# Kernel tuning notes

Hardware: AMD Instinct MI355X
Metric: run time of the kernel (lower is better)

## Reference

```python
import jax, jax.numpy as jnp
import numpy as np

EPS = 1e-6
HEADS = 4


def _gather(x, idx):
    # x: (b,n,...), idx: (b,n,k) -> (b,n,k,...)
    return jax.vmap(lambda xb, ib: xb[ib])(x, idx)


def _prenorm(f0, f1):
    # FiberNorm: layernorm on scalars, norm-based RMS normalization on vectors
    mu = jnp.mean(f0, -1, keepdims=True)
    var = jnp.var(f0, -1, keepdims=True)
    g0 = (f0 - mu) * jax.lax.rsqrt(var + EPS)
    n1 = jnp.sum(f1 * f1, -1)  # (b,n,d1) squared channel norms
    rms = jax.lax.rsqrt(jnp.mean(n1, -1, keepdims=True) + EPS)  # (b,n,1)
    g1 = f1 * rms[..., None]
    return g0, g1


def _forward(f0, f1, coords, nbr_idx, Wq0, Wq1, Wk00, Wk10, Wk01, Wk11, Wk11r,
             Wv00, Wv10, Wv01, Wv11, Wv11r, Rw1, Rb1, Rw20, Rw21, Wo0, Wo1,
             F0w1, F0w2, F1w1, F1w2):
    b, n, d0 = f0.shape
    d1 = f1.shape[2]
    k = nbr_idx.shape[-1]
    L = Wq0.shape[0]
    # equivariant basis ingredients: relative positions over neighbor graph
    rel = _gather(coords, nbr_idx) - coords[:, :, None, :]       # (b,n,k,3)
    dist = jnp.linalg.norm(rel, axis=-1, keepdims=True)          # (b,n,k,1)
    rhat = rel / (dist + EPS)                                    # (b,n,k,3)
    scale = 1.0 / np.sqrt(d0 // HEADS + 3 * (d1 // HEADS)).astype(np.float32)
    for l in range(L):
        # ---- attention block (prenorm -> TFN attention -> residual) ----
        g0, g1 = _prenorm(f0, f1)
        rh = jax.nn.gelu(dist @ Rw1[l] + Rb1[l])                 # radial MLP (b,n,k,rh)
        r0 = rh @ Rw20[l]                                        # (b,n,k,d0)
        r1 = rh @ Rw21[l]                                        # (b,n,k,d1)
        q0 = g0 @ Wq0[l]                                         # (b,n,d0)
        q1 = jnp.einsum('bncm,ce->bnem', g1, Wq1[l])             # (b,n,d1,3)
        h0 = _gather(g0, nbr_idx)                                # (b,n,k,d0)
        h1 = _gather(g1, nbr_idx)                                # (b,n,k,d1,3)
        dot1 = jnp.einsum('bnkcm,bnkm->bnkc', h1, rhat)          # deg1->deg0 basis contraction
        k0 = (h0 @ Wk00[l] + dot1 @ Wk10[l]) * r0
        v0 = (h0 @ Wv00[l] + dot1 @ Wv10[l]) * r0
        rh_e = rhat[:, :, :, None, :]                            # (b,n,k,1,3)
        k1 = (jnp.einsum('bnkc,ce->bnke', h0, Wk01[l])[..., None] * rh_e
              + jnp.einsum('bnkcm,ce->bnkem', h1, Wk11[l])
              + jnp.einsum('bnkc,ce->bnke', dot1, Wk11r[l])[..., None] * rh_e) * r1[..., None]
        v1 = (jnp.einsum('bnkc,ce->bnke', h0, Wv01[l])[..., None] * rh_e
              + jnp.einsum('bnkcm,ce->bnkem', h1, Wv11[l])
              + jnp.einsum('bnkc,ce->bnke', dot1, Wv11r[l])[..., None] * rh_e) * r1[..., None]
        # multi-head invariant attention logits over neighbors
        hq0 = q0.reshape(b, n, HEADS, -1)
        hk0 = k0.reshape(b, n, k, HEADS, -1)
        hq1 = q1.reshape(b, n, HEADS, -1, 3)
        hk1 = k1.reshape(b, n, k, HEADS, -1, 3)
        logits = (jnp.einsum('bnhc,bnkhc->bnkh', hq0, hk0)
                  + jnp.einsum('bnhcm,bnkhcm->bnkh', hq1, hk1)) * scale
        a = jax.nn.softmax(logits, axis=2)                       # over neighbors
        o0 = jnp.einsum('bnkh,bnkhc->bnhc', a, v0.reshape(b, n, k, HEADS, -1)).reshape(b, n, d0)
        o1 = jnp.einsum('bnkh,bnkhcm->bnhcm', a, v1.reshape(b, n, k, HEADS, -1, 3)).reshape(b, n, d1, 3)
        f0 = f0 + o0 @ Wo0[l]
        f1 = f1 + jnp.einsum('bncm,ce->bnem', o1, Wo1[l])
        # ---- feedforward residual block (prenorm -> fiber FF -> residual) ----
        g0, g1 = _prenorm(f0, f1)
        f0 = f0 + jax.nn.gelu(g0 @ F0w1[l]) @ F0w2[l]
        u1 = jnp.einsum('bncm,ce->bnem', g1, F1w1[l])            # (b,n,4*d1,3)
        gate = jax.nn.sigmoid(jnp.linalg.norm(u1, axis=-1))     # norm-gated equivariant nonlin
        u1 = u1 * gate[..., None]
        f1 = f1 + jnp.einsum('bnem,ef->bnfm', u1, F1w2[l])
    return jnp.concatenate([f0, f1.reshape(b, n, d1 * 3)], axis=-1)


def setup_inputs() -> dict:
    key = jax.random.key(0)
    ks = iter(jax.random.split(key, 40))
    b, n, k, d0, d1, L, rh = 2, 4096, 32, 64, 16, 2, 16
    def w(shape, fan):
        return jax.random.normal(next(ks), shape, jnp.float32) / np.sqrt(fan).astype(np.float32)
    inp = {
        'f0': jax.random.normal(next(ks), (b, n, d0), jnp.float32),
        'f1': jax.random.normal(next(ks), (b, n, d1, 3), jnp.float32),
        'coords': jax.random.normal(next(ks), (b, n, 3), jnp.float32),
        'nbr_idx': jax.random.randint(next(ks), (b, n, k), 0, n),
        'Wq0': w((L, d0, d0), d0), 'Wq1': w((L, d1, d1), d1),
        'Wk00': w((L, d0, d0), d0), 'Wk10': w((L, d1, d0), d1),
        'Wk01': w((L, d0, d1), d0), 'Wk11': w((L, d1, d1), d1), 'Wk11r': w((L, d1, d1), d1),
        'Wv00': w((L, d0, d0), d0), 'Wv10': w((L, d1, d0), d1),
        'Wv01': w((L, d0, d1), d0), 'Wv11': w((L, d1, d1), d1), 'Wv11r': w((L, d1, d1), d1),
        'Rw1': w((L, 1, rh), 1), 'Rb1': jnp.zeros((L, rh), jnp.float32),
        'Rw20': w((L, rh, d0), rh), 'Rw21': w((L, rh, d1), rh),
        'Wo0': w((L, d0, d0), d0), 'Wo1': w((L, d1, d1), d1),
        'F0w1': w((L, d0, 4 * d0), d0), 'F0w2': w((L, 4 * d0, d0), 4 * d0),
        'F1w1': w((L, d1, 4 * d1), d1), 'F1w2': w((L, 4 * d1, d1), 4 * d1),
    }
    return inp


def reference(f0, f1, coords, nbr_idx, Wq0, Wq1, Wk00, Wk10, Wk01, Wk11, Wk11r,
              Wv00, Wv10, Wv01, Wv11, Wv11r, Rw1, Rb1, Rw20, Rw21, Wo0, Wo1,
              F0w1, F0w2, F1w1, F1w2):
    return _forward(f0, f1, coords, nbr_idx, Wq0, Wq1, Wk00, Wk10, Wk01, Wk11,
                    Wk11r, Wv00, Wv10, Wv01, Wv11, Wv11r, Rw1, Rb1, Rw20, Rw21,
                    Wo0, Wo1, F0w1, F0w2, F1w1, F1w2)
```

## Files before the change

### kernel.cpp

```cpp
#include <hip/hip_runtime.h>
#include <math.h>

#define BB    2
#define NN    4096
#define KK    32
#define D0    64
#define D1    16
#define D13   48
#define RHD   16
#define NHEAD 4
#define NLAYER 2
#define EPS   1e-6f
#define SCALE 0.18898223650461363f
#define ETOT  (BB*NN*KK)

typedef float  f32x4 __attribute__((ext_vector_type(4)));
typedef short  s16x8 __attribute__((ext_vector_type(8)));
#define MFMA16(a,b,c) __builtin_amdgcn_mfma_f32_16x16x32_bf16(a,b,c,0,0,0)

__device__ __forceinline__ unsigned short f2bf(float x) {
    union { float f; unsigned u; } v; v.f = x;
    unsigned r = v.u + 0x7fffu + ((v.u >> 16) & 1u);
    return (unsigned short)(r >> 16);
}
__device__ __forceinline__ float bf2f(unsigned short h) {
    union { unsigned u; float f; } v; v.u = ((unsigned)h) << 16;
    return v.f;
}
__device__ __forceinline__ void split_bf(float x, unsigned short* hi, unsigned short* lo) {
    unsigned short h = f2bf(x);
    *hi = h;
    *lo = f2bf(x - bf2f(h));
}

__device__ __forceinline__ f32x4 mm3(s16x8 ah, s16x8 al, s16x8 bh, s16x8 bl, f32x4 c) {
    c = MFMA16(ah, bh, c);
    c = MFMA16(ah, bl, c);
    c = MFMA16(al, bh, c);
    return c;
}

__device__ __forceinline__ float wred(float v) {
    #pragma unroll
    for (int o = 32; o > 0; o >>= 1) v += __shfl_xor(v, o, 64);
    return v;
}

__device__ __forceinline__ float gelu_t(float x) {
    float x3 = x * x * x;
    return 0.5f * x * (1.0f + tanhf(0.7978845608028654f * (x + 0.044715f * x3)));
}

__global__ void geom_kernel(const float* __restrict__ coords,
                            const int* __restrict__ nbr,
                            float* __restrict__ rhat,
                            float* __restrict__ dist) {
    int e = blockIdx.x * blockDim.x + threadIdx.x;
    if (e >= ETOT) return;
    int bn = e / KK;
    int bb = bn / NN;
    int j  = nbr[e];
    const float* cs = coords + (size_t)bn * 3;
    const float* cn = coords + ((size_t)bb * NN + j) * 3;
    float rx = cn[0] - cs[0], ry = cn[1] - cs[1], rz = cn[2] - cs[2];
    float d  = sqrtf(rx * rx + ry * ry + rz * rz);
    float iv = 1.0f / (d + EPS);
    rhat[e * 3 + 0] = rx * iv;
    rhat[e * 3 + 1] = ry * iv;
    rhat[e * 3 + 2] = rz * iv;
    dist[e] = d;
}

__global__ __launch_bounds__(64) void prenorm_q_kernel(
    const float* __restrict__ f0, const float* __restrict__ f1,
    const float* __restrict__ Wq0, const float* __restrict__ Wq1,
    float* __restrict__ g1,
    float* __restrict__ q0, float* __restrict__ q1,
    unsigned short* __restrict__ g0H, unsigned short* __restrict__ g0L,
    unsigned short* __restrict__ g1mH, unsigned short* __restrict__ g1mL) {
    int node = blockIdx.x;
    int lane = threadIdx.x;
    __shared__ float g0s[D0], g1s[D13];

    float x  = f0[(size_t)node * D0 + lane];
    float mu = wred(x) * (1.0f / D0);
    float dv = x - mu;
    float var = wred(dv * dv) * (1.0f / D0);
    float g0v = dv * rsqrtf(var + EPS);
    split_bf(g0v, &g0H[(size_t)node * D0 + lane], &g0L[(size_t)node * D0 + lane]);
    g0s[lane] = g0v;

    float w = (lane < D13) ? f1[(size_t)node * D13 + lane] : 0.0f;
    float t = wred(w * w);
    float rms = rsqrtf(t * (1.0f / D1) + EPS);
    if (lane < D13) {
        float g1v = w * rms;
        g1[(size_t)node * D13 + lane] = g1v;
        g1s[lane] = g1v;
        int c = lane / 3, m = lane % 3;
        split_bf(g1v, &g1mH[(size_t)node * D13 + m * 16 + c],
                      &g1mL[(size_t)node * D13 + m * 16 + c]);
    }
    __syncthreads();

    float acc = 0.0f;
    #pragma unroll
    for (int c = 0; c < D0; c++) acc += g0s[c] * Wq0[c * D0 + lane];
    q0[(size_t)node * D0 + lane] = acc;
    if (lane < D13) {
        int e = lane / 3, m = lane % 3;
        float a1 = 0.0f;
        #pragma unroll
        for (int c = 0; c < D1; c++) a1 += g1s[c * 3 + m] * Wq1[c * D1 + e];
        q1[(size_t)node * D13 + lane] = a1;
    }
}

__global__ __launch_bounds__(256) void edge_prep_kernel(
    const int* __restrict__ nbr,
    const float* __restrict__ rhatb, const float* __restrict__ distb,
    const float* __restrict__ g1b,
    const float* __restrict__ Rw1, const float* __restrict__ Rb1,
    unsigned short* __restrict__ d1H, unsigned short* __restrict__ d1L,
    unsigned short* __restrict__ rhHg, unsigned short* __restrict__ rhLg) {
    int t = blockIdx.x * 256 + threadIdx.x;
    int e = t >> 4, c = t & 15;
    int bn = e >> 5;
    int bb = bn >> 12;
    int nj = nbr[e];
    const float* g1 = g1b + ((size_t)bb * NN + nj) * D13 + c * 3;
    float d1 = g1[0] * rhatb[e * 3] + g1[1] * rhatb[e * 3 + 1] + g1[2] * rhatb[e * 3 + 2];
    split_bf(d1, &d1H[t], &d1L[t]);
    float rh = gelu_t(distb[e] * Rw1[c] + Rb1[c]);
    split_bf(rh, &rhHg[t], &rhLg[t]);
}

__device__ __forceinline__ float B1val(int n, int k,
    const float* Wk00, const float* Wk10, const float* Wv00, const float* Wv10) {
    int nn = n & 63;
    const float* W0 = (n < 64) ? Wk00 : Wv00;
    const float* W1 = (n < 64) ? Wk10 : Wv10;
    if (k < 64) return W0[k * D0 + nn];
    if (k < 80) return W1[(k - 64) * D0 + nn];
    return 0.0f;
}
__device__ __forceinline__ float B2val(int n, int k,
    const float* Wk01, const float* Wk11, const float* Wk11r,
    const float* Wv01, const float* Wv11, const float* Wv11r) {
    if (n < 16) {
        if (k < 64) return Wk01[k * D1 + n];
        if (k < 80) return Wk11r[(k - 64) * D1 + n];
        return 0.0f;
    }
    if (n < 32) {
        int e = n - 16;
        if (k < 64) return Wv01[k * D1 + e];
        if (k < 80) return Wv11r[(k - 64) * D1 + e];
        return 0.0f;
    }
    if (n < 80) {
        int m = (n - 32) >> 4, e = (n - 32) & 15;
        if (k >= 80) { int mm = (k - 80) >> 4, c = (k - 80) & 15; if (mm == m) return Wk11[c * D1 + e]; }
        return 0.0f;
    }
    { int m = (n - 80) >> 4, e = (n - 80) & 15;
      if (k >= 80) { int mm = (k - 80) >> 4, c = (k - 80) & 15; if (mm == m) return Wv11[c * D1 + e]; }
      return 0.0f; }
}

__global__ void prep_kernel(
    const float* __restrict__ Wk00, const float* __restrict__ Wk10,
    const float* __restrict__ Wk01, const float* __restrict__ Wk11,
    const float* __restrict__ Wk11r,
    const float* __restrict__ Wv00, const float* __restrict__ Wv10,
    const float* __restrict__ Wv01, const float* __restrict__ Wv11,
    const float* __restrict__ Wv11r,
    const float* __restrict__ Rw20, const float* __restrict__ Rw21,
    unsigned short* __restrict__ B1H, unsigned short* __restrict__ B1L,
    unsigned short* __restrict__ B2H, unsigned short* __restrict__ B2L,
    unsigned short* __restrict__ R0H, unsigned short* __restrict__ R0L,
    unsigned short* __restrict__ R1H, unsigned short* __restrict__ R1L) {
    int id = blockIdx.x * 256 + threadIdx.x;
    if (id < 1536) {
        int ks = id >> 9, rem = id & 511, nt = rem >> 6, lane = rem & 63;
        int li = lane & 15, quad = lane >> 4;
        #pragma unroll
        for (int t = 0; t < 8; t++) {
            float v = B1val(nt * 16 + li, ks * 32 + quad * 8 + t, Wk00, Wk10, Wv00, Wv10);
            split_bf(v, &B1H[id * 8 + t], &B1L[id * 8 + t]);
        }
    } else if (id < 3584) {
        int id2 = id - 1536;
        int ks = id2 >> 9, rem = id2 & 511, nt = rem >> 6, lane = rem & 63;
        int li = lane & 15, quad = lane >> 4;
        #pragma unroll
        for (int t = 0; t < 8; t++) {
            float v = B2val(nt * 16 + li, ks * 32 + quad * 8 + t,
                            Wk01, Wk11, Wk11r, Wv01, Wv11, Wv11r);
            split_bf(v, &B2H[id2 * 8 + t], &B2L[id2 * 8 + t]);
        }
    } else if (id < 3840) {
        int id2 = id - 3584;
        int nt = id2 >> 6, lane = id2 & 63;
        int li = lane & 15, quad = lane >> 4;
        #pragma unroll
        for (int t = 0; t < 8; t++) {
            int k = quad * 8 + t;
            float v = (k < 16) ? Rw20[k * D0 + nt * 16 + li] : 0.0f;
            split_bf(v, &R0H[id2 * 8 + t], &R0L[id2 * 8 + t]);
        }
    } else if (id < 3904) {
        int id2 = id - 3840;
        int li = id2 & 15, quad = id2 >> 4;
        #pragma unroll
        for (int t = 0; t < 8; t++) {
            int k = quad * 8 + t;
            float v = (k < 16) ? Rw21[k * D1 + li] : 0.0f;
            split_bf(v, &R1H[id2 * 8 + t], &R1L[id2 * 8 + t]);
        }
    }
}

__global__ __launch_bounds__(64) void attn_fused_kernel(
    const int* __restrict__ nbr_idx,
    const float* __restrict__ rhatg,
    const float* __restrict__ q0g, const float* __restrict__ q1g,
    const unsigned short* __restrict__ g0H, const unsigned short* __restrict__ g0L,
    const unsigned short* __restrict__ g1mH, const unsigned short* __restrict__ g1mL,
    const unsigned short* __restrict__ d1H, const unsigned short* __restrict__ d1L,
    const unsigned short* __restrict__ rhHg, const unsigned short* __restrict__ rhLg,
    const unsigned short* __restrict__ B1H, const unsigned short* __restrict__ B1L,
    const unsigned short* __restrict__ B2H, const unsigned short* __restrict__ B2L,
    const unsigned short* __restrict__ R0H, const unsigned short* __restrict__ R0L,
    const unsigned short* __restrict__ R1H, const unsigned short* __restrict__ R1L,
    const float* __restrict__ Wo0, const float* __restrict__ Wo1,
    float* __restrict__ f0b, float* __restrict__ f1b) {

    int B0    = blockIdx.x * 64;
    int node0 = blockIdx.x * 2;
    int bb    = node0 >> 12;
    int lane  = threadIdx.x;
    int li    = lane & 15, quad = lane >> 4;
    int koff  = quad * 8;

    __shared__ float rhts[192];
    __shared__ float lgs0[64][4];
    __shared__ float lgs1[64][4];
    __shared__ float v0s[64][68];
    __shared__ float v1s[64][49];
    __shared__ float o0s[2][D0];
    __shared__ float o1s[2][D13];

    rhts[lane]       = rhatg[(size_t)B0 * 3 + lane];
    rhts[lane + 64]  = rhatg[(size_t)B0 * 3 + lane + 64];
    rhts[lane + 128] = rhatg[(size_t)B0 * 3 + lane + 128];
    __syncthreads();

    size_t em[4], nm[4];
    #pragma unroll
    for (int mt = 0; mt < 4; mt++) {
        em[mt] = (size_t)B0 + mt * 16 + li;
        nm[mt] = (size_t)bb * NN + nbr_idx[em[mt]];
    }

    #define APTRS(ks, nb, ee, PH, PL)                                              \
        const unsigned short *PH, *PL;                                             \
        if (ks < 2) {                                                              \
            PH = g0H + (nb) * 64 + ks * 32 + koff;                                 \
            PL = g0L + (nb) * 64 + ks * 32 + koff;                                 \
        } else if (ks == 2) {                                                      \
            PH = (quad < 2) ? d1H + (ee) * 16 + quad * 8                           \
                            : g1mH + (nb) * 48 + (quad - 2) * 8;                   \
            PL = (quad < 2) ? d1L + (ee) * 16 + quad * 8                           \
                            : g1mL + (nb) * 48 + (quad - 2) * 8;                   \
        } else {                                                                   \
            PH = (quad < 2) ? g1mH + (nb) * 48 + 16 + quad * 8                     \
                            : g1mH + (nb) * 48 + 32 + (quad - 2) * 8;              \
            PL = (quad < 2) ? g1mL + (nb) * 48 + 16 + quad * 8                     \
                            : g1mL + (nb) * 48 + 32 + (quad - 2) * 8;              \
        }

    f32x4 acc[4][8];

    #pragma unroll
    for (int i = 0; i < 4; i++)
        #pragma unroll
        for (int j = 0; j < 8; j++) acc[i][j] = (f32x4){0.f, 0.f, 0.f, 0.f};
    #pragma unroll
    for (int ks = 0; ks < 3; ks++) {
        s16x8 ah[4], al[4];
        #pragma unroll
        for (int mt = 0; mt < 4; mt++) {
            APTRS(ks, nm[mt], em[mt], pH, pL)
            ah[mt] = *(const s16x8*)pH;
            al[mt] = *(const s16x8*)pL;
        }
        #pragma unroll
        for (int nt = 0; nt < 8; nt++) {
            s16x8 bh = *(const s16x8*)(B1H + ((ks * 8 + nt) * 64 + lane) * 8);
            s16x8 bl = *(const s16x8*)(B1L + ((ks * 8 + nt) * 64 + lane) * 8);
            #pragma unroll
            for (int mt = 0; mt < 4; mt++)
                acc[mt][nt] = mm3(ah[mt], al[mt], bh, bl, acc[mt][nt]);
        }
    }

    {
        f32x4 r0a[4][4];
        #pragma unroll
        for (int i = 0; i < 4; i++)
            #pragma unroll
            for (int j = 0; j < 4; j++) r0a[i][j] = (f32x4){0.f, 0.f, 0.f, 0.f};
        s16x8 zz = (s16x8){0,0,0,0,0,0,0,0};
        s16x8 rah[4], ral[4];
        #pragma unroll
        for (int mt = 0; mt < 4; mt++) {
            rah[mt] = zz; ral[mt] = zz;
            if (quad < 2) {
                rah[mt] = *(const s16x8*)(rhHg + em[mt] * 16 + koff);
                ral[mt] = *(const s16x8*)(rhLg + em[mt] * 16 + koff);
            }
        }
        #pragma unroll
        for (int nt = 0; nt < 4; nt++) {
            s16x8 bh = *(const s16x8*)(R0H + (nt * 64 + lane) * 8);
            s16x8 bl = *(const s16x8*)(R0L + (nt * 64 + lane) * 8);
            #pragma unroll
            for (int mt = 0; mt < 4; mt++)
                r0a[mt][nt] = mm3(rah[mt], ral[mt], bh, bl, r0a[mt][nt]);
        }

        float q0e[2][4];
        #pragma unroll
        for (int nw = 0; nw < 2; nw++)
            #pragma unroll
            for (int nt = 0; nt < 4; nt++)
                q0e[nw][nt] = q0g[(size_t)(node0 + nw) * D0 + nt * 16 + li];
        #pragma unroll
        for (int mt = 0; mt < 4; mt++) {
            int nw = mt >> 1;
            float p0[4][4];
            #pragma unroll
            for (int nt = 0; nt < 4; nt++)
                #pragma unroll
                for (int r = 0; r < 4; r++)
                    p0[nt][r] = q0e[nw][nt] * (acc[mt][nt][r] * r0a[mt][nt][r]);
            #pragma unroll
            for (int off = 1; off < 16; off <<= 1) {
                #pragma unroll
                for (int nt = 0; nt < 4; nt++)
                    #pragma unroll
                    for (int r = 0; r < 4; r++)
                        p0[nt][r] += __shfl_xor(p0[nt][r], off, 16);
            }
            if (li == 0) {
                int jb = mt * 16 + quad * 4;
                #pragma unroll
                for (int r = 0; r < 4; r++)
                    #pragma unroll
                    for (int nt = 0; nt < 4; nt++)
                        lgs0[jb + r][nt] = p0[nt][r];
            }
            #pragma unroll
            for (int nt = 0; nt < 4; nt++)
                #pragma unroll
                for (int r = 0; r < 4; r++)
                    v0s[mt * 16 + quad * 4 + r][nt * 16 + li] =
                        acc[mt][nt + 4][r] * r0a[mt][nt][r];
        }
    }

    f32x4 r1a[4];
    {
        s16x8 zz = (s16x8){0,0,0,0,0,0,0,0};
        s16x8 bh = *(const s16x8*)(R1H + lane * 8);
        s16x8 bl = *(const s16x8*)(R1L + lane * 8);
        #pragma unroll
        for (int mt = 0; mt < 4; mt++) {
            s16x8 rah = zz, ral = zz;
            if (quad < 2) {
                rah = *(const s16x8*)(rhHg + em[mt] * 16 + koff);
                ral = *(const s16x8*)(rhLg + em[mt] * 16 + koff);
            }
            r1a[mt] = (f32x4){0.f, 0.f, 0.f, 0.f};
            r1a[mt] = mm3(rah, ral, bh, bl, r1a[mt]);
        }
    }

    #pragma unroll
    for (int i = 0; i < 4; i++)
        #pragma unroll
        for (int j = 0; j < 8; j++) acc[i][j] = (f32x4){0.f, 0.f, 0.f, 0.f};
    #pragma unroll
    for (int ks = 0; ks < 4; ks++) {
        s16x8 ah[4], al[4];
        #pragma unroll
        for (int mt = 0; mt < 4; mt++) {
            APTRS(ks, nm[mt], em[mt], pH, pL)
            ah[mt] = *(const s16x8*)pH;
            al[mt] = *(const s16x8*)pL;
        }
        #pragma unroll
        for (int nt = 0; nt < 8; nt++) {
            s16x8 bh = *(const s16x8*)(B2H + ((ks * 8 + nt) * 64 + lane) * 8);
            s16x8 bl = *(const s16x8*)(B2L + ((ks * 8 + nt) * 64 + lane) * 8);
            #pragma unroll
            for (int mt = 0; mt < 4; mt++)
                acc[mt][nt] = mm3(ah[mt], al[mt], bh, bl, acc[mt][nt]);
        }
    }

    {
        float q1v[2][3];
        #pragma unroll
        for (int nw = 0; nw < 2; nw++)
            #pragma unroll
            for (int m = 0; m < 3; m++)
                q1v[nw][m] = q1g[(size_t)(node0 + nw) * D13 + li * 3 + m];
        #pragma unroll
        for (int mt = 0; mt < 4; mt++) {
            int nw = mt >> 1;
            #pragma unroll
            for (int r = 0; r < 4; r++) {
                int j = mt * 16 + quad * 4 + r;
                float r1  = r1a[mt][r];
                float rh0 = rhts[j * 3], rh1 = rhts[j * 3 + 1], rh2 = rhts[j * 3 + 2];
                float sk = acc[mt][0][r], sv = acc[mt][1][r];
                float k1a = (sk * rh0 + acc[mt][2][r]) * r1;
                float k1b = (sk * rh1 + acc[mt][3][r]) * r1;
                float k1c = (sk * rh2 + acc[mt][4][r]) * r1;
                v1s[j][li * 3 + 0] = (sv * rh0 + acc[mt][5][r]) * r1;
                v1s[j][li * 3 + 1] = (sv * rh1 + acc[mt][6][r]) * r1;
                v1s[j][li * 3 + 2] = (sv * rh2 + acc[mt][7][r]) * r1;
                float lc = q1v[nw][0] * k1a + q1v[nw][1] * k1b + q1v[nw][2] * k1c;
                lc += __shfl_xor(lc, 1, 4);
                lc += __shfl_xor(lc, 2, 4);
                if ((li & 3) == 0) lgs1[j][li >> 2] = lc;
            }
        }
    }
    __syncthreads();

    {
        float4 a4 = *(const float4*)&lgs0[lane][0];
        float4 b4 = *(const float4*)&lgs1[lane][0];
        float4 l4;
        l4.x = (a4.x + b4.x) * SCALE; l4.y = (a4.y + b4.y) * SCALE;
        l4.z = (a4.z + b4.z) * SCALE; l4.w = (a4.w + b4.w) * SCALE;
        float4 mx = l4;
        #pragma unroll
        for (int off = 1; off < 32; off <<= 1) {
            mx.x = fmaxf(mx.x, __shfl_xor(mx.x, off, 32));
            mx.y = fmaxf(mx.y, __shfl_xor(mx.y, off, 32));
            mx.z = fmaxf(mx.z, __shfl_xor(mx.z, off, 32));
            mx.w = fmaxf(mx.w, __shfl_xor(mx.w, off, 32));
        }
        float4 ex;
        ex.x = expf(l4.x - mx.x); ex.y = expf(l4.y - mx.y);
        ex.z = expf(l4.z - mx.z); ex.w = expf(l4.w - mx.w);
        float4 s = ex;
        #pragma unroll
        for (int off = 1; off < 32; off <<= 1) {
            s.x += __shfl_xor(s.x, off, 32);
            s.y += __shfl_xor(s.y, off, 32);
            s.z += __shfl_xor(s.z, off, 32);
            s.w += __shfl_xor(s.w, off, 32);
        }
        ex.x /= s.x; ex.y /= s.y; ex.z /= s.z; ex.w /= s.w;
        *(float4*)&lgs0[lane][0] = ex;
    }
    __syncthreads();

    {
        int h0 = lane >> 4;
        #pragma unroll
        for (int nw = 0; nw < 2; nw++) {
            float p = 0.0f;
            #pragma unroll
            for (int jn = 0; jn < KK; jn++)
                p += lgs0[nw * 32 + jn][h0] * v0s[nw * 32 + jn][lane];
            o0s[nw][lane] = p;
        }
    }
    if (lane < D13) {
        int h1 = (lane / 3) >> 2;
        #pragma unroll
        for (int nw = 0; nw < 2; nw++) {
            float p = 0.0f;
            #pragma unroll
            for (int jn = 0; jn < KK; jn++)
                p += lgs0[nw * 32 + jn][h1] * v1s[nw * 32 + jn][lane];
            o1s[nw][lane] = p;
        }
    }
    __syncthreads();

    #pragma unroll
    for (int nw = 0; nw < 2; nw++) {
        float a0 = 0.0f;
        #pragma unroll
        for (int e = 0; e < D0; e++) a0 += o0s[nw][e] * Wo0[e * D0 + lane];
        f0b[(size_t)(node0 + nw) * D0 + lane] += a0;
    }
    if (lane < D13) {
        int f = lane / 3, m = lane % 3;
        #pragma unroll
        for (int nw = 0; nw < 2; nw++) {
            float a1 = 0.0f;
            #pragma unroll
            for (int c = 0; c < D1; c++) a1 += o1s[nw][c * 3 + m] * Wo1[c * D1 + f];
            f1b[(size_t)(node0 + nw) * D13 + lane] += a1;
        }
    }
    #undef APTRS
}

__global__ __launch_bounds__(256) void ffn_kernel(
    const float* __restrict__ F0w1, const float* __restrict__ F0w2,
    const float* __restrict__ F1w1, const float* __restrict__ F1w2,
    float* __restrict__ f0b, float* __restrict__ f1b) {
    int w    = threadIdx.x >> 6, lane = threadIdx.x & 63;
    int node = blockIdx.x * 4 + w;

    __shared__ float g0s[4][D0];
    __shared__ float g1s[4][D13];
    __shared__ float ts[4][256];
    __shared__ float us[4][192];

    {
        float x  = f0b[(size_t)node * D0 + lane];
        float mu = wred(x) * (1.0f / D0);
        float dv = x - mu;
        float var = wred(dv * dv) * (1.0f / D0);
        g0s[w][lane] = dv * rsqrtf(var + EPS);

        float ww = (lane < D13) ? f1b[(size_t)node * D13 + lane] : 0.0f;
        float t = wred(ww * ww);
        float rms = rsqrtf(t * (1.0f / D1) + EPS);
        if (lane < D13) g1s[w][lane] = ww * rms;
    }
    __syncthreads();

    #pragma unroll
    for (int u = 0; u < 4; u++) {
        int h = u * 64 + lane;
        float acc = 0.0f;
        #pragma unroll
        for (int c = 0; c < D0; c++) acc += g0s[w][c] * F0w1[c * 256 + h];
        ts[w][h] = gelu_t(acc);
    }
    #pragma unroll
    for (int u = 0; u < 3; u++) {
        int t = u * 64 + lane;
        int e = t / 3, m = t % 3;
        float acc = 0.0f;
        #pragma unroll
        for (int c = 0; c < D1; c++) acc += g1s[w][c * 3 + m] * F1w1[c * 64 + e];
        us[w][t] = acc;
    }
    __syncthreads();

    {
        float a = us[w][lane * 3], b = us[w][lane * 3 + 1], c = us[w][lane * 3 + 2];
        float nrm = sqrtf(a * a + b * b + c * c);
        float gate = 1.0f / (1.0f + expf(-nrm));
        us[w][lane * 3 + 0] = a * gate;
        us[w][lane * 3 + 1] = b * gate;
        us[w][lane * 3 + 2] = c * gate;
    }
    __syncthreads();

    {
        float acc = 0.0f;
        #pragma unroll 8
        for (int j = 0; j < 256; j++) acc += ts[w][j] * F0w2[j * D0 + lane];
        f0b[(size_t)node * D0 + lane] += acc;
    }
    if (lane < D13) {
        int f = lane / 3, m = lane % 3;
        float acc = 0.0f;
        #pragma unroll
        for (int e = 0; e < 64; e++) acc += us[w][e * 3 + m] * F1w2[e * D1 + f];
        f1b[(size_t)node * D13 + lane] += acc;
    }
}

__global__ void concat_kernel(const float* __restrict__ f0b,
                              const float* __restrict__ f1b,
                              float* __restrict__ out) {
    int i = blockIdx.x * blockDim.x + threadIdx.x;
    if (i >= BB * NN * (D0 + D13)) return;
    int node = i / (D0 + D13), c = i % (D0 + D13);
    out[i] = (c < D0) ? f0b[(size_t)node * D0 + c]
                      : f1b[(size_t)node * D13 + (c - D0)];
}

extern "C" void kernel_launch(void* const* d_in, const int* in_sizes, int n_in,
                              void* d_out, int out_size, void* d_ws, size_t ws_size,
                              hipStream_t stream) {
    const float* f0     = (const float*)d_in[0];
    const float* f1     = (const float*)d_in[1];
    const float* coords = (const float*)d_in[2];
    const int*   nbr    = (const int*)d_in[3];
    const float* Wq0    = (const float*)d_in[4];
    const float* Wq1    = (const float*)d_in[5];
    const float* Wk00   = (const float*)d_in[6];
    const float* Wk10   = (const float*)d_in[7];
    const float* Wk01   = (const float*)d_in[8];
    const float* Wk11   = (const float*)d_in[9];
    const float* Wk11r  = (const float*)d_in[10];
    const float* Wv00   = (const float*)d_in[11];
    const float* Wv10   = (const float*)d_in[12];
    const float* Wv01   = (const float*)d_in[13];
    const float* Wv11   = (const float*)d_in[14];
    const float* Wv11r  = (const float*)d_in[15];
    const float* Rw1    = (const float*)d_in[16];
    const float* Rb1    = (const float*)d_in[17];
    const float* Rw20   = (const float*)d_in[18];
    const float* Rw21   = (const float*)d_in[19];
    const float* Wo0    = (const float*)d_in[20];
    const float* Wo1    = (const float*)d_in[21];
    const float* F0w1   = (const float*)d_in[22];
    const float* F0w2   = (const float*)d_in[23];
    const float* F1w1   = (const float*)d_in[24];
    const float* F1w2   = (const float*)d_in[25];
    float* out = (float*)d_out;

    int nodes = BB * NN;

    float* wf = (float*)d_ws;
    float* f0b   = wf; wf += (size_t)nodes * D0;
    float* f1b   = wf; wf += (size_t)nodes * D13;
    float* g1b   = wf; wf += (size_t)nodes * D13;
    float* q0b   = wf; wf += (size_t)nodes * D0;
    float* q1b   = wf; wf += (size_t)nodes * D13;
    float* rhatb = wf; wf += (size_t)ETOT * 3;
    float* distb = wf; wf += (size_t)ETOT;
    unsigned short* wu = (unsigned short*)wf;
    unsigned short* g0H  = wu; wu += (size_t)nodes * D0;
    unsigned short* g0L  = wu; wu += (size_t)nodes * D0;
    unsigned short* g1mH = wu; wu += (size_t)nodes * D13;
    unsigned short* g1mL = wu; wu += (size_t)nodes * D13;
    unsigned short* d1H  = wu; wu += (size_t)ETOT * 16;
    unsigned short* d1L  = wu; wu += (size_t)ETOT * 16;
    unsigned short* rhH  = wu; wu += (size_t)ETOT * 16;
    unsigned short* rhL  = wu; wu += (size_t)ETOT * 16;
    unsigned short* B1H = wu; wu += 1536 * 8;
    unsigned short* B1L = wu; wu += 1536 * 8;
    unsigned short* B2H = wu; wu += 2048 * 8;
    unsigned short* B2L = wu; wu += 2048 * 8;
    unsigned short* R0H = wu; wu += 256 * 8;
    unsigned short* R0L = wu; wu += 256 * 8;
    unsigned short* R1H = wu; wu += 64 * 8;
    unsigned short* R1L = wu; wu += 64 * 8;

    geom_kernel<<<(ETOT + 255) / 256, 256, 0, stream>>>(coords, nbr, rhatb, distb);
    hipMemcpyAsync(f0b, f0, (size_t)nodes * D0 * sizeof(float),
                   hipMemcpyDeviceToDevice, stream);
    hipMemcpyAsync(f1b, f1, (size_t)nodes * D13 * sizeof(float),
                   hipMemcpyDeviceToDevice, stream);

    for (int l = 0; l < NLAYER; l++) {
        prenorm_q_kernel<<<nodes, 64, 0, stream>>>(
            f0b, f1b, Wq0 + l * D0 * D0, Wq1 + l * D1 * D1,
            g1b, q0b, q1b, g0H, g0L, g1mH, g1mL);
        prep_kernel<<<16, 256, 0, stream>>>(
            Wk00 + l * D0 * D0, Wk10 + l * D1 * D0,
            Wk01 + l * D0 * D1, Wk11 + l * D1 * D1, Wk11r + l * D1 * D1,
            Wv00 + l * D0 * D0, Wv10 + l * D1 * D0,
            Wv01 + l * D0 * D1, Wv11 + l * D1 * D1, Wv11r + l * D1 * D1,
            Rw20 + l * RHD * D0, Rw21 + l * RHD * D1,
            B1H, B1L, B2H, B2L, R0H, R0L, R1H, R1L);
        edge_prep_kernel<<<ETOT * 16 / 256, 256, 0, stream>>>(
            nbr, rhatb, distb, g1b, Rw1 + l * RHD, Rb1 + l * RHD,
            d1H, d1L, rhH, rhL);
        attn_fused_kernel<<<ETOT / 64, 64, 0, stream>>>(
            nbr, rhatb, q0b, q1b,
            g0H, g0L, g1mH, g1mL, d1H, d1L, rhH, rhL,
            B1H, B1L, B2H, B2L, R0H, R0L, R1H, R1L,
            Wo0 + l * D0 * D0, Wo1 + l * D1 * D1,
            f0b, f1b);
        ffn_kernel<<<nodes / 4, 256, 0, stream>>>(
            F0w1 + l * D0 * 256, F0w2 + l * 256 * D0,
            F1w1 + l * D1 * 64, F1w2 + l * 64 * D1,
            f0b, f1b);
    }

    concat_kernel<<<(nodes * (D0 + D13) + 255) / 256, 256, 0, stream>>>(f0b, f1b, out);
}
```

Baseline: 458.8 us.

## Fuse next-layer prenorm/Q into FFN, batch weight prep, fold concat into FFN

Weight preprocessing for both layers now runs in a single launch before the layer loop. The FFN kernel also computes the next layer's prenorm and Q projections, and on the last layer writes the concatenated output directly. Together these drop the per-layer prenorm_q and prep launches and the separate concat kernel, saving launch overhead and a re-read of node features. The cost is a heavier FFN kernel with an extra sync and more parameters.

```diff
diff --git a/kernel.cpp b/kernel.cpp
--- a/kernel.cpp
+++ b/kernel.cpp
@@ -180,14 +180,38 @@
     unsigned short* __restrict__ B2H, unsigned short* __restrict__ B2L,
     unsigned short* __restrict__ R0H, unsigned short* __restrict__ R0L,
     unsigned short* __restrict__ R1H, unsigned short* __restrict__ R1L) {
-    int id = blockIdx.x * 256 + threadIdx.x;
+    int gid = blockIdx.x * 256 + threadIdx.x;
+    if (gid >= 2 * 3904) return;
+    int l  = (gid >= 3904) ? 1 : 0;
+    int id = gid - l * 3904;
+    const float* Wk00l = Wk00 + l * D0 * D0;
+    const float* Wk10l = Wk10 + l * D1 * D0;
+    const float* Wk01l = Wk01 + l * D0 * D1;
+    const float* Wk11l = Wk11 + l * D1 * D1;
+    const float* Wk11rl= Wk11r+ l * D1 * D1;
+    const float* Wv00l = Wv00 + l * D0 * D0;
+    const float* Wv10l = Wv10 + l * D1 * D0;
+    const float* Wv01l = Wv01 + l * D0 * D1;
+    const float* Wv11l = Wv11 + l * D1 * D1;
+    const float* Wv11rl= Wv11r+ l * D1 * D1;
+    const float* Rw20l = Rw20 + l * RHD * D0;
+    const float* Rw21l = Rw21 + l * RHD * D1;
+    unsigned short* B1Hl = B1H + l * 1536 * 8;
+    unsigned short* B1Ll = B1L + l * 1536 * 8;
+    unsigned short* B2Hl = B2H + l * 2048 * 8;
+    unsigned short* B2Ll = B2L + l * 2048 * 8;
+    unsigned short* R0Hl = R0H + l * 256 * 8;
+    unsigned short* R0Ll = R0L + l * 256 * 8;
+    unsigned short* R1Hl = R1H + l * 64 * 8;
+    unsigned short* R1Ll = R1L + l * 64 * 8;
+
     if (id < 1536) {
         int ks = id >> 9, rem = id & 511, nt = rem >> 6, lane = rem & 63;
         int li = lane & 15, quad = lane >> 4;
         #pragma unroll
         for (int t = 0; t < 8; t++) {
-            float v = B1val(nt * 16 + li, ks * 32 + quad * 8 + t, Wk00, Wk10, Wv00, Wv10);
-            split_bf(v, &B1H[id * 8 + t], &B1L[id * 8 + t]);
+            float v = B1val(nt * 16 + li, ks * 32 + quad * 8 + t, Wk00l, Wk10l, Wv00l, Wv10l);
+            split_bf(v, &B1Hl[id * 8 + t], &B1Ll[id * 8 + t]);
         }
     } else if (id < 3584) {
         int id2 = id - 1536;
@@ -196,8 +220,8 @@
         #pragma unroll
         for (int t = 0; t < 8; t++) {
             float v = B2val(nt * 16 + li, ks * 32 + quad * 8 + t,
-                            Wk01, Wk11, Wk11r, Wv01, Wv11, Wv11r);
-            split_bf(v, &B2H[id2 * 8 + t], &B2L[id2 * 8 + t]);
+                            Wk01l, Wk11l, Wk11rl, Wv01l, Wv11l, Wv11rl);
+            split_bf(v, &B2Hl[id2 * 8 + t], &B2Ll[id2 * 8 + t]);
         }
     } else if (id < 3840) {
         int id2 = id - 3584;
@@ -206,17 +230,17 @@
         #pragma unroll
         for (int t = 0; t < 8; t++) {
             int k = quad * 8 + t;
-            float v = (k < 16) ? Rw20[k * D0 + nt * 16 + li] : 0.0f;
-            split_bf(v, &R0H[id2 * 8 + t], &R0L[id2 * 8 + t]);
-        }
-    } else if (id < 3904) {
+            float v = (k < 16) ? Rw20l[k * D0 + nt * 16 + li] : 0.0f;
+            split_bf(v, &R0Hl[id2 * 8 + t], &R0Ll[id2 * 8 + t]);
+        }
+    } else {
         int id2 = id - 3840;
         int li = id2 & 15, quad = id2 >> 4;
         #pragma unroll
         for (int t = 0; t < 8; t++) {
             int k = quad * 8 + t;
-            float v = (k < 16) ? Rw21[k * D1 + li] : 0.0f;
-            split_bf(v, &R1H[id2 * 8 + t], &R1L[id2 * 8 + t]);
+            float v = (k < 16) ? Rw21l[k * D1 + li] : 0.0f;
+            split_bf(v, &R1Hl[id2 * 8 + t], &R1Ll[id2 * 8 + t]);
         }
     }
 }
@@ -518,7 +542,13 @@
 __global__ __launch_bounds__(256) void ffn_kernel(
     const float* __restrict__ F0w1, const float* __restrict__ F0w2,
     const float* __restrict__ F1w1, const float* __restrict__ F1w2,
-    float* __restrict__ f0b, float* __restrict__ f1b) {
+    float* __restrict__ f0b, float* __restrict__ f1b,
+    int last,
+    const float* __restrict__ Wq0n, const float* __restrict__ Wq1n,
+    float* __restrict__ g1b, float* __restrict__ q0b, float* __restrict__ q1b,
+    unsigned short* __restrict__ g0H, unsigned short* __restrict__ g0L,
+    unsigned short* __restrict__ g1mH, unsigned short* __restrict__ g1mL,
+    float* __restrict__ out) {
     int w    = threadIdx.x >> 6, lane = threadIdx.x & 63;
     int node = blockIdx.x * 4 + w;
 
@@ -527,17 +557,18 @@
     __shared__ float ts[4][256];
     __shared__ float us[4][192];
 
-    {
-        float x  = f0b[(size_t)node * D0 + lane];
-        float mu = wred(x) * (1.0f / D0);
-        float dv = x - mu;
+    float f0old = f0b[(size_t)node * D0 + lane];
+    float f1old = (lane < D13) ? f1b[(size_t)node * D13 + lane] : 0.0f;
+
+    {
+        float mu = wred(f0old) * (1.0f / D0);
+        float dv = f0old - mu;
         float var = wred(dv * dv) * (1.0f / D0);
         g0s[w][lane] = dv * rsqrtf(var + EPS);
 
-        float ww = (lane < D13) ? f1b[(size_t)node * D13 + lane] : 0.0f;
-        float t = wred(ww * ww);
+        float t = wred(f1old * f1old);
         float rms = rsqrtf(t * (1.0f / D1) + EPS);
-        if (lane < D13) g1s[w][lane] = ww * rms;
+        if (lane < D13) g1s[w][lane] = f1old * rms;
     }
     __syncthreads();
 
@@ -570,29 +601,63 @@
     }
     __syncthreads();
 
+    float f0new;
     {
         float acc = 0.0f;
         #pragma unroll 8
         for (int j = 0; j < 256; j++) acc += ts[w][j] * F0w2[j * D0 + lane];
-        f0b[(size_t)node * D0 + lane] += acc;
-    }
+        f0new = f0old + acc;
+    }
+    float f1new = f1old;
     if (lane < D13) {
         int f = lane / 3, m = lane % 3;
         float acc = 0.0f;
         #pragma unroll
         for (int e = 0; e < 64; e++) acc += us[w][e * 3 + m] * F1w2[e * D1 + f];
-        f1b[(size_t)node * D13 + lane] += acc;
-    }
-}
-
-__global__ void concat_kernel(const float* __restrict__ f0b,
-                              const float* __restrict__ f1b,
-                              float* __restrict__ out) {
-    int i = blockIdx.x * blockDim.x + threadIdx.x;
-    if (i >= BB * NN * (D0 + D13)) return;
-    int node = i / (D0 + D13), c = i % (D0 + D13);
-    out[i] = (c < D0) ? f0b[(size_t)node * D0 + c]
-                      : f1b[(size_t)node * D13 + (c - D0)];
+        f1new = f1old + acc;
+    }
+
+    if (last) {
+        out[(size_t)node * (D0 + D13) + lane] = f0new;
+        if (lane < D13) out[(size_t)node * (D0 + D13) + D0 + lane] = f1new;
+        return;
+    }
+
+    f0b[(size_t)node * D0 + lane] = f0new;
+    if (lane < D13) f1b[(size_t)node * D13 + lane] = f1new;
+
+    float mu = wred(f0new) * (1.0f / D0);
+    float dv = f0new - mu;
+    float var = wred(dv * dv) * (1.0f / D0);
+    float g0v = dv * rsqrtf(var + EPS);
+    split_bf(g0v, &g0H[(size_t)node * D0 + lane], &g0L[(size_t)node * D0 + lane]);
+    float w1v = (lane < D13) ? f1new : 0.0f;
+    float t2 = wred(w1v * w1v);
+    float rms2 = rsqrtf(t2 * (1.0f / D1) + EPS);
+    g0s[w][lane] = g0v;
+    if (lane < D13) {
+        float g1v = w1v * rms2;
+        g1b[(size_t)node * D13 + lane] = g1v;
+        g1s[w][lane] = g1v;
+        int c = lane / 3, m = lane % 3;
+        split_bf(g1v, &g1mH[(size_t)node * D13 + m * 16 + c],
+                      &g1mL[(size_t)node * D13 + m * 16 + c]);
+    }
+    __syncthreads();
+
+    {
+        float acc = 0.0f;
+        #pragma unroll
+        for (int c = 0; c < D0; c++) acc += g0s[w][c] * Wq0n[c * D0 + lane];
+        q0b[(size_t)node * D0 + lane] = acc;
+    }
+    if (lane < D13) {
+        int e = lane / 3, m = lane % 3;
+        float a1 = 0.0f;
+        #pragma unroll
+        for (int c = 0; c < D1; c++) a1 += g1s[w][c * 3 + m] * Wq1n[c * D1 + e];
+        q1b[(size_t)node * D13 + lane] = a1;
+    }
 }
 
 extern "C" void kernel_launch(void* const* d_in, const int* in_sizes, int n_in,
@@ -645,14 +710,14 @@
     unsigned short* d1L  = wu; wu += (size_t)ETOT * 16;
     unsigned short* rhH  = wu; wu += (size_t)ETOT * 16;
     unsigned short* rhL  = wu; wu += (size_t)ETOT * 16;
-    unsigned short* B1H = wu; wu += 1536 * 8;
-    unsigned short* B1L = wu; wu += 1536 * 8;
-    unsigned short* B2H = wu; wu += 2048 * 8;
-    unsigned short* B2L = wu; wu += 2048 * 8;
-    unsigned short* R0H = wu; wu += 256 * 8;
-    unsigned short* R0L = wu; wu += 256 * 8;
-    unsigned short* R1H = wu; wu += 64 * 8;
-    unsigned short* R1L = wu; wu += 64 * 8;
+    unsigned short* B1H = wu; wu += 2 * 1536 * 8;
+    unsigned short* B1L = wu; wu += 2 * 1536 * 8;
+    unsigned short* B2H = wu; wu += 2 * 2048 * 8;
+    unsigned short* B2L = wu; wu += 2 * 2048 * 8;
+    unsigned short* R0H = wu; wu += 2 * 256 * 8;
+    unsigned short* R0L = wu; wu += 2 * 256 * 8;
+    unsigned short* R1H = wu; wu += 2 * 64 * 8;
+    unsigned short* R1L = wu; wu += 2 * 64 * 8;
 
     geom_kernel<<<(ETOT + 255) / 256, 256, 0, stream>>>(coords, nbr, rhatb, distb);
     hipMemcpyAsync(f0b, f0, (size_t)nodes * D0 * sizeof(float),
@@ -660,31 +725,33 @@
     hipMemcpyAsync(f1b, f1, (size_t)nodes * D13 * sizeof(float),
                    hipMemcpyDeviceToDevice, stream);
 
+    prep_kernel<<<(2 * 3904 + 255) / 256, 256, 0, stream>>>(
+        Wk00, Wk10, Wk01, Wk11, Wk11r, Wv00, Wv10, Wv01, Wv11, Wv11r,
+        Rw20, Rw21, B1H, B1L, B2H, B2L, R0H, R0L, R1H, R1L);
+
+    prenorm_q_kernel<<<nodes, 64, 0, stream>>>(
+        f0b, f1b, Wq0, Wq1, g1b, q0b, q1b, g0H, g0L, g1mH, g1mL);
+
     for (int l = 0; l < NLAYER; l++) {
-        prenorm_q_kernel<<<nodes, 64, 0, stream>>>(
-            f0b, f1b, Wq0 + l * D0 * D0, Wq1 + l * D1 * D1,
-            g1b, q0b, q1b, g0H, g0L, g1mH, g1mL);
-        prep_kernel<<<16, 256, 0, stream>>>(
-            Wk00 + l * D0 * D0, Wk10 + l * D1 * D0,
-            Wk01 + l * D0 * D1, Wk11 + l * D1 * D1, Wk11r + l * D1 * D1,
-            Wv00 + l * D0 * D0, Wv10 + l * D1 * D0,
-            Wv01 + l * D0 * D1, Wv11 + l * D1 * D1, Wv11r + l * D1 * D1,
-            Rw20 + l * RHD * D0, Rw21 + l * RHD * D1,
-            B1H, B1L, B2H, B2L, R0H, R0L, R1H, R1L);
+        int last = (l == NLAYER - 1);
+        int ln   = last ? 0 : (l + 1);
         edge_prep_kernel<<<ETOT * 16 / 256, 256, 0, stream>>>(
             nbr, rhatb, distb, g1b, Rw1 + l * RHD, Rb1 + l * RHD,
             d1H, d1L, rhH, rhL);
         attn_fused_kernel<<<ETOT / 64, 64, 0, stream>>>(
             nbr, rhatb, q0b, q1b,
             g0H, g0L, g1mH, g1mL, d1H, d1L, rhH, rhL,
-            B1H, B1L, B2H, B2L, R0H, R0L, R1H, R1L,
+            B1H + l * 1536 * 8, B1L + l * 1536 * 8,
+            B2H + l * 2048 * 8, B2L + l * 2048 * 8,
+            R0H + l * 256 * 8,  R0L + l * 256 * 8,
+            R1H + l * 64 * 8,   R1L + l * 64 * 8,
             Wo0 + l * D0 * D0, Wo1 + l * D1 * D1,
             f0b, f1b);
         ffn_kernel<<<nodes / 4, 256, 0, stream>>>(
             F0w1 + l * D0 * 256, F0w2 + l * 256 * D0,
             F1w1 + l * D1 * 64, F1w2 + l * 64 * D1,
-            f0b, f1b);
-    }
-
-    concat_kernel<<<(nodes * (D0 + D13) + 255) / 256, 256, 0, stream>>>(f0b, f1b, out);
-}
+            f0b, f1b, last,
+            Wq0 + ln * D0 * D0, Wq1 + ln * D1 * D1,
+            g1b, q0b, q1b, g0H, g0L, g1mH, g1mL, out);
+    }
+}
```

Measured after the change: 450.8 us (median of 3 runs). About the same (-1.7%).
